# Kernel tuning notes

Measured on AMD Instinct MI355X. Metric: run time of the kernel, lower is better.

## Reference

```python
import jax, jax.numpy as jnp
import numpy as np

B, N, M = 2, 4096, 12288
K, SH, H, GK, NC, F = 64, 32, 64, 8, 200, 1


def sph_to_cart(theta, phi):
    st = jnp.sin(theta)
    return jnp.stack([st * jnp.cos(phi), st * jnp.sin(phi), jnp.cos(theta)], axis=-1)


def setup_inputs() -> dict:
    key = jax.random.key(0)
    ks = jax.random.split(key, 16)
    theta = jax.random.uniform(ks[0], (B, N)) * jnp.pi
    phi = jax.random.uniform(ks[1], (B, N)) * 2 * jnp.pi
    feat = jax.random.normal(ks[2], (B, N))
    xxx = jnp.stack([theta, phi, feat], axis=1)  # [B,3,N]
    pt = jax.random.uniform(ks[3], (M,)) * jnp.pi
    pp = jax.random.uniform(ks[4], (M,)) * 2 * jnp.pi
    pix_theta_phi = jnp.stack([pt, pp], axis=1)  # [M,2]
    s = 0.1
    return dict(
        xxx=xxx,
        pix_theta_phi=pix_theta_phi,
        att_w1=jax.random.normal(ks[5], (F + 1, SH)) * s,
        att_b1=jnp.zeros((SH,)),
        att_w2=jax.random.normal(ks[6], (SH, 1)) * s,
        att_b2=jnp.zeros((1,)),
        proj_w=jax.random.normal(ks[7], (F, H)) * s,
        proj_b=jnp.zeros((H,)),
        rel_w=jax.random.normal(ks[8], (3, H, H)) * s,
        rel_b=jnp.zeros((3, H)),
        root_w=jax.random.normal(ks[9], (3, H, H)) * s,
        out_w1=jax.random.normal(ks[10], (H, H)) * s,
        out_b1=jnp.zeros((H,)),
        out_w2=jax.random.normal(ks[11], (H, NC)) * s,
        out_b2=jnp.zeros((NC,)),
    )


def reference(xxx, pix_theta_phi, att_w1, att_b1, att_w2, att_b2, proj_w, proj_b,
              rel_w, rel_b, root_w, out_w1, out_b1, out_w2, out_b2):
    # --- sparse healpix sampler ---
    los_tp = jnp.transpose(xxx[:, :2, :], (0, 2, 1))   # [B,N,2]
    x = xxx[:, 2, :][..., None]                        # [B,N,1]
    r_los = sph_to_cart(los_tp[..., 0], los_tp[..., 1])           # [B,N,3]
    r_pix = sph_to_cart(pix_theta_phi[:, 0], pix_theta_phi[:, 1])  # [M,3]
    cos = jnp.clip(jnp.einsum('bnc,mc->bmn', r_los, r_pix), -1.0, 1.0)  # [B,M,N]
    vals, idx = jax.lax.top_k(cos, K)                  # [B,M,K]
    x_g = jax.vmap(lambda xb, ib: xb[ib])(x, idx)      # [B,M,K,F]
    d = jnp.arccos(jnp.clip(vals, -1.0, 1.0))          # [B,M,K]
    feat = jnp.concatenate([x_g, d[..., None]], axis=-1)  # [B,M,K,F+1]
    logits = jax.nn.relu(feat @ att_w1 + att_b1) @ att_w2 + att_b2  # [B,M,K,1]
    w = jax.nn.softmax(logits[..., 0], axis=-1)        # [B,M,K]
    pooled = jnp.einsum('bmk,bmkf->bmf', w, x_g)       # [B,M,F]
    # --- GNN on healpix grid ---
    h = jax.nn.relu(pooled @ proj_w + proj_b)          # [B,M,H]
    m = r_pix.shape[0]
    sq = jnp.sum(r_pix * r_pix, axis=1)
    d2 = sq[:, None] + sq[None, :] - 2.0 * (r_pix @ r_pix.T)       # [M,M]
    d2 = jnp.where(jnp.eye(m, dtype=bool), jnp.inf, d2)  # loop=False
    _, nbr = jax.lax.top_k(-d2, GK)                    # [M,GK] knn_graph
    for i in range(rel_w.shape[0]):
        agg = h[:, nbr, :].sum(axis=2)                 # sum-aggregate neighbor msgs
        h = jax.nn.relu(agg @ rel_w[i] + rel_b[i] + h @ root_w[i])
    graph_feat = h.mean(axis=1)                        # global_mean_pool -> [B,H]
    out = jax.nn.relu(graph_feat @ out_w1 + out_b1) @ out_w2 + out_b2
    return out
```

## Files before the change

### kernel.cpp

```cpp
#include <hip/hip_runtime.h>
#include <hip/hip_bf16.h>

#define B_ 2
#define N_ 4096
#define M_ 12288
#define K_ 64
#define SH_ 32
#define H_ 64
#define GK_ 8
#define NC_ 200

#define KCAP 128
#define BCAP2 48
#define SCAP 192
#define MG_ 0.01f
#define C256_ 81.48733086f

static __device__ __forceinline__ unsigned f2key(float f) {
  unsigned b = __float_as_uint(f);
  return (b & 0x80000000u) ? ~b : (b | 0x80000000u);
}
static __device__ __forceinline__ float key2f(unsigned u) {
  unsigned b = (u & 0x80000000u) ? (u & 0x7fffffffu) : ~u;
  return __uint_as_float(b);
}
static __device__ __forceinline__ unsigned long long shflxor64(unsigned long long x, int m) {
  unsigned lo = (unsigned)x, hi = (unsigned)(x >> 32);
  lo = (unsigned)__shfl_xor((int)lo, m);
  hi = (unsigned)__shfl_xor((int)hi, m);
  return ((unsigned long long)hi << 32) | lo;
}
static __device__ __forceinline__ unsigned long long kpack(float s, int j) {
  return ((unsigned long long)f2key(s) << 14) | (unsigned)(16383 - j);
}
static __device__ __forceinline__ unsigned long long spack(float c, int n) {
  return ((unsigned long long)f2key(c) << 12) | (unsigned)(4095 - n);
}
static __device__ __forceinline__ int thbkt(float th) {
  int b = (int)(th * C256_);
  return b < 0 ? 0 : (b > 255 ? 255 : b);
}
static __device__ __forceinline__ float clamp1(float x) { return fminf(1.f, fmaxf(-1.f, x)); }
static __device__ __forceinline__ float rdlane(float v, int c) {
  return __uint_as_float((unsigned)__builtin_amdgcn_readlane((int)__float_as_uint(v), c));
}

__global__ __launch_bounds__(256) void sentinel_vF(float* out, int n, float val) {
  int t = blockIdx.x * 256 + threadIdx.x;
  if (t < n) out[t] = val;
}

#define GRIDB_ 129
#define PREPN_ (M_ + B_*N_ + B_*H_)
#define PREPB_ ((PREPN_ + 255)/256)

__global__ __launch_bounds__(256) void prep_vF(
    const float* __restrict__ xxx, const float* __restrict__ pix,
    float4* __restrict__ r_pix, float4* __restrict__ r_los, float* __restrict__ gf,
    float* __restrict__ kthrG, float* __restrict__ cthrG, unsigned* __restrict__ cnt)
{
  const float PI = 3.14159265358979f;
  if ((int)blockIdx.x < GRIDB_) {
    int gid  = blockIdx.x*4 + (threadIdx.x >> 6);
    if (gid >= 514) return;
    int lane = threadIdx.x & 63;
    int tgt  = (gid >= 257) ? 1 : 0;
    int gp   = gid - tgt*257;
    float thp = (float)gp * (PI/256.f);
    float cp = cosf(thp), sp = fmaxf(sinf(thp), 1e-6f);
    float thq = ((float)lane + 0.5f) * (PI/64.f);
    float sq = sinf(thq), cq = cosf(thq);
    float rinv = 1.0f / (sq * sp);
    float At = tgt ? (2.f*PI*PI*128.f/(float)N_) : (2.f*PI*PI*48.f/(float)M_);
    float lo = 1e-3f, hi = 3.1414f;
    for (int it = 0; it < 12; ++it) {
      float al = 0.5f*(lo + hi);
      float ca = cosf(al);
      float arg = clamp1((ca - cq*cp) * rinv);
      float ax = fabsf(arg);
      float ac = sqrtf(fmaxf(0.f, 1.f - ax)) *
                 fmaf(ax, fmaf(ax, fmaf(ax, -0.0187293f, 0.0742610f), -0.2121144f), 1.5707288f);
      ac = (arg < 0.f) ? (PI - ac) : ac;
      float S = ac;
      #pragma unroll
      for (int off = 32; off; off >>= 1) S += __shfl_xor(S, off);
      float A = 2.f * S * (PI/64.f);
      if (A < At) lo = al; else hi = al;
    }
    if (lane == 0) {
      float chv = cosf(hi);
      if (tgt) cthrG[gp] = chv - 1e-5f;
      else     kthrG[gp] = 2.f*chv - 1.00002f;
    }
  } else {
    int tid = ((int)blockIdx.x - GRIDB_)*256 + threadIdx.x;
    if (tid < M_) {
      float th = pix[2*tid], ph = pix[2*tid+1];
      float st = sinf(th);
      float x = st*cosf(ph), y = st*sinf(ph), z = cosf(th);
      r_pix[tid] = make_float4(x, y, z, x*x + y*y + z*z);
      atomicAdd(&cnt[thbkt(th)], 1u);
    }
    int t2 = tid - M_;
    if (t2 >= 0 && t2 < B_*N_) {
      int b = t2 >> 12, n = t2 & (N_-1);
      const float* xb = xxx + b*3*N_;
      float th = xb[n], ph = xb[N_+n], ft = xb[2*N_+n];
      float st = sinf(th);
      r_los[t2] = make_float4(st*cosf(ph), st*sinf(ph), cosf(th), ft);
      atomicAdd(&cnt[256 + b*256 + thbkt(th)], 1u);
    }
    int t3 = tid - M_ - B_*N_;
    if (t3 >= 0 && t3 < B_*H_) gf[t3] = 0.0f;
  }
}

__global__ __launch_bounds__(256) void scan_vF(
    const unsigned* __restrict__ cnt, int* __restrict__ pstart, int* __restrict__ lstart,
    unsigned* __restrict__ pcur, unsigned* __restrict__ lcur)
{
  __shared__ unsigned buf[256];
  const int t = threadIdx.x;
  for (int arr = 0; arr < 3; ++arr) {
    unsigned v = cnt[arr*256 + t];
    buf[t] = v;
    __syncthreads();
    for (int off = 1; off < 256; off <<= 1) {
      unsigned o = (t >= off) ? buf[t - off] : 0u;
      __syncthreads();
      buf[t] += o;
      __syncthreads();
    }
    unsigned incl = buf[t], excl = incl - v;
    if (arr == 0) {
      pstart[t] = (int)excl; if (t == 255) pstart[256] = (int)incl;
      pcur[t] = excl;
    } else {
      int b = arr - 1;
      lstart[b*257 + t] = (int)excl; if (t == 255) lstart[b*257 + 256] = (int)incl;
      lcur[b*256 + t] = excl;
    }
    __syncthreads();
  }
}

__global__ __launch_bounds__(256) void scatter_vF(
    const float* __restrict__ xxx, const float* __restrict__ pix,
    const float4* __restrict__ r_pix, const float4* __restrict__ r_los,
    unsigned* __restrict__ pcur, unsigned* __restrict__ lcur,
    float4* __restrict__ spix, int* __restrict__ sjdx,
    float4* __restrict__ slos, int* __restrict__ sldx)
{
  int tid = blockIdx.x * 256 + threadIdx.x;
  if (tid < M_) {
    int bkt = thbkt(pix[2*tid]);
    unsigned pos = atomicAdd(&pcur[bkt], 1u);
    spix[pos] = r_pix[tid];
    sjdx[pos] = tid;
  } else {
    int t2 = tid - M_;
    if (t2 < B_*N_) {
      int b = t2 >> 12, n = t2 & (N_-1);
      int bkt = thbkt(xxx[b*3*N_ + n]);
      unsigned pos = atomicAdd(&lcur[b*256 + bkt], 1u);
      slos[b*N_ + pos] = r_los[t2];
      sldx[b*N_ + pos] = n;
    }
  }
}

__global__ __launch_bounds__(512) void sampler_vF(
    const float* __restrict__ pix,
    const float4* __restrict__ spix, const int* __restrict__ sjdx,
    const float4* __restrict__ slos, const int* __restrict__ sldx,
    const int* __restrict__ lstart, const float4* __restrict__ r_los,
    const float* __restrict__ cthrG,
    const float* __restrict__ aw1, const float* __restrict__ ab1,
    const float* __restrict__ aw2, const float* __restrict__ ab2,
    float* __restrict__ pooled)
{
  __shared__ unsigned long long cand[16][SCAP];
  __shared__ unsigned long long selKey[16][K_];
  __shared__ unsigned long long bndK[16][BCAP2];
  __shared__ unsigned hist[16][64];

  const int tid = threadIdx.x, wv = tid >> 6, lane = tid & 63;
  const int b  = blockIdx.y;
  const int srow0 = blockIdx.x*16 + wv*2, srow1 = srow0 + 1;
  const int r0 = wv*2, r1 = r0 + 1;
  const int m0 = sjdx[srow0], m1 = sjdx[srow1];
  const float4 p0 = spix[srow0], p1 = spix[srow1];
  const float thp0 = pix[2*m0], thp1 = pix[2*m1];
  const int g0 = thbkt(thp0), g1 = thbkt(thp1);
  const float th0 = fminf(cthrG[g0], cthrG[g0+1]);
  const float th1 = fminf(cthrG[g1], cthrG[g1+1]);
  const float inv0 = 63.999f / (1.000001f - th0);
  const float inv1 = 63.999f / (1.000001f - th1);
  const float4* sl = slos + b * N_;
  const int* sx = sldx + b * N_;
  const float4* rl = r_los + b * N_;
  const int* ls = lstart + b * 257;
  const unsigned long long ltm = (1ull << lane) - 1ull;

  int jlo, jhi;
  {
    float al0 = acosf(clamp1(th0)), al1 = acosf(clamp1(th1));
    int blo = thbkt(fminf(thp0 - al0, thp1 - al1) - MG_);
    int bhi = thbkt(fmaxf(thp0 + al0, thp1 + al1) + MG_);
    jlo = ls[blo]; jhi = ls[bhi + 1];
  }

  unsigned cnt0 = 0, cnt1 = 0;
  for (int base = jlo; base < jhi; base += 64) {
    int pos = base + lane;
    bool act = pos < jhi;
    float c0 = -2.f, c1 = -2.f; int n = 0;
    if (act) {
      float4 v = sl[pos]; n = sx[pos];
      c0 = clamp1(v.x*p0.x + v.y*p0.y + v.z*p0.z);
      c1 = clamp1(v.x*p1.x + v.y*p1.y + v.z*p1.z);
    }
    bool pr0 = c0 > th0, pr1 = c1 > th1;
    unsigned long long mk0 = __ballot(pr0);
    if (mk0) {
      unsigned off = (unsigned)__popcll(mk0 & ltm);
      if (pr0 && cnt0 + off < SCAP) cand[r0][cnt0 + off] = spack(c0, n);
      cnt0 += (unsigned)__popcll(mk0);
    }
    unsigned long long mk1 = __ballot(pr1);
    if (mk1) {
      unsigned off = (unsigned)__popcll(mk1 & ltm);
      if (pr1 && cnt1 + off < SCAP) cand[r1][cnt1 + off] = spack(c1, n);
      cnt1 += (unsigned)__popcll(mk1);
    }
  }

  for (int rr = 0; rr < 2; ++rr) {
    const int r = (rr == 0) ? r0 : r1;
    const int m = (rr == 0) ? m0 : m1;
    const float4 p = (rr == 0) ? p0 : p1;
    const float thp = (rr == 0) ? thp0 : thp1;
    const float thg = (rr == 0) ? th0 : th1;
    const float invg = (rr == 0) ? inv0 : inv1;
    unsigned cn = (rr == 0) ? cnt0 : cnt1;
    bool fin = false;

    if (cn >= (unsigned)K_ && cn <= (unsigned)SCAP) {
      hist[r][lane] = 0u;
      for (int i = lane; i < (int)cn; i += 64) {
        float c = key2f((unsigned)(cand[r][i] >> 12));
        atomicAdd(&hist[r][(int)((c - thg) * invg)], 1u);
      }
      unsigned g = hist[r][lane], s = g;
      #pragma unroll
      for (int off = 1; off < 64; off <<= 1) {
        unsigned t2 = (unsigned)__shfl_down((int)s, off);
        s += (lane + off < 64) ? t2 : 0u;
      }
      unsigned snext = s - g;
      unsigned packed = (s >= K_ && snext < K_) ? (((unsigned)(lane+1) << 16) | snext) : 0u;
      #pragma unroll
      for (int off = 32; off; off >>= 1) {
        unsigned o = (unsigned)__shfl_xor((int)packed, off);
        packed = packed > o ? packed : o;
      }
      const int t = (int)(packed >> 16) - 1;
      const unsigned chi = packed & 0xFFFFu;
      const unsigned need = K_ - chi;

      unsigned hiC = 0, bdC = 0;
      for (int i0 = 0; i0 < (int)cn; i0 += 64) {
        int i = i0 + lane;
        bool act = i < (int)cn;
        unsigned long long key = act ? cand[r][i] : 0ull;
        int bin = -1;
        if (act) bin = (int)((key2f((unsigned)(key >> 12)) - thg) * invg);
        bool pHi = act && bin > t, pBd = act && bin == t;
        unsigned long long mH = __ballot(pHi);
        unsigned offH = (unsigned)__popcll(mH & ltm);
        if (pHi && hiC + offH < K_) selKey[r][hiC + offH] = key;
        hiC += (unsigned)__popcll(mH);
        unsigned long long mB = __ballot(pBd);
        unsigned offB = (unsigned)__popcll(mB & ltm);
        if (pBd && bdC + offB < BCAP2) bndK[r][bdC + offB] = key;
        bdC += (unsigned)__popcll(mB);
      }
      if (bdC <= (unsigned)BCAP2) {
        if (lane < (int)bdC) {
          unsigned long long ki = bndK[r][lane];
          int rank = 0;
          for (int j = 0; j < (int)bdC; ++j) rank += (bndK[r][j] > ki) ? 1 : 0;
          if ((unsigned)rank < need) selKey[r][chi + rank] = ki;
        }
        fin = true;
      }
    }

    if (!fin) {
      float th = thg;
      float inv = invg;
      int wlo = jlo, whi = jhi;

      if (cn >= (unsigned)K_) {
        hist[r][lane] = 0u;
        cn = 0;
        for (int base = wlo; base < whi; base += 64) {
          int pos = base + lane;
          bool act = pos < whi;
          float c = -2.f;
          if (act) {
            float4 v = sl[pos];
            c = clamp1(v.x*p.x + v.y*p.y + v.z*p.z);
          }
          bool pr = c > th;
          if (pr) atomicAdd(&hist[r][(int)((c - th) * inv)], 1u);
          cn += (unsigned)__popcll(__ballot(pr));
        }
      }

      int tries = 0;
      while (cn < K_ && tries < 3) {
        th = 1.f - 1.6f*(1.f - th); ++tries;
        inv = 63.999f / (1.000001f - th);
        float al = acosf(clamp1(th));
        int blo = thbkt(thp - al - MG_), bhi = thbkt(thp + al + MG_);
        wlo = ls[blo]; whi = ls[bhi + 1];
        hist[r][lane] = 0u;
        cn = 0;
        for (int base = wlo; base < whi; base += 64) {
          int pos = base + lane;
          bool act = pos < whi;
          float c = -2.f;
          if (act) {
            float4 v = sl[pos];
            c = clamp1(v.x*p.x + v.y*p.y + v.z*p.z);
          }
          bool pr = c > th;
          if (pr) atomicAdd(&hist[r][(int)((c - th) * inv)], 1u);
          cn += (unsigned)__popcll(__ballot(pr));
        }
      }

      bool fin2 = false;
      if (cn >= K_) {
        unsigned g = hist[r][lane], s = g;
        #pragma unroll
        for (int off = 1; off < 64; off <<= 1) {
          unsigned t2 = (unsigned)__shfl_down((int)s, off);
          s += (lane + off < 64) ? t2 : 0u;
        }
        unsigned snext = s - g;
        unsigned packed = (s >= K_ && snext < K_) ? (((unsigned)(lane+1) << 16) | snext) : 0u;
        #pragma unroll
        for (int off = 32; off; off >>= 1) {
          unsigned o = (unsigned)__shfl_xor((int)packed, off);
          packed = packed > o ? packed : o;
        }
        const int t = (int)(packed >> 16) - 1;
        const unsigned chi = packed & 0xFFFFu;
        const unsigned need = K_ - chi;

        unsigned hiC = 0, bdC = 0;
        for (int base = wlo; base < whi; base += 64) {
          int pos = base + lane;
          bool act = pos < whi;
          float c = -2.f; int n = 0;
          if (act) {
            float4 v = sl[pos]; n = sx[pos];
            c = clamp1(v.x*p.x + v.y*p.y + v.z*p.z);
          }
          int bin = (act && c > th) ? (int)((c - th) * inv) : -1;
          bool pHi = bin > t;
          bool pBd = bin == t;
          unsigned long long mH = __ballot(pHi);
          unsigned offH = (unsigned)__popcll(mH & ltm);
          if (pHi && hiC + offH < K_) selKey[r][hiC + offH] = spack(c, n);
          hiC += (unsigned)__popcll(mH);
          unsigned long long mB = __ballot(pBd);
          unsigned offB = (unsigned)__popcll(mB & ltm);
          if (pBd && bdC + offB < BCAP2) bndK[r][bdC + offB] = spack(c, n);
          bdC += (unsigned)__popcll(mB);
        }
        if (bdC <= (unsigned)BCAP2) {
          if (lane < (int)bdC) {
            unsigned long long ki = bndK[r][lane];
            int rank = 0;
            for (int j = 0; j < (int)bdC; ++j) rank += (bndK[r][j] > ki) ? 1 : 0;
            if ((unsigned)rank < need) selKey[r][chi + rank] = ki;
          }
          fin2 = true;
        }
      }

      if (!fin2) {
        unsigned long long prev = ~0ull;
        for (int rd = 0; rd < K_; ++rd) {
          unsigned long long best = 0ull;
          for (int i = 0; i < 64; ++i) {
            int n = lane + 64*i;
            float4 v = rl[n];
            float c = clamp1(v.x*p.x + v.y*p.y + v.z*p.z);
            unsigned long long k = spack(c, n);
            if (k < prev && k > best) best = k;
          }
          #pragma unroll
          for (int off = 1; off < 64; off <<= 1) {
            unsigned long long o = shflxor64(best, off);
            best = o > best ? o : best;
          }
          if (lane == 0) selKey[r][rd] = best;
          prev = best;
        }
      }
    }

    {
      unsigned long long key = selKey[r][lane];
      int n = 4095 - (int)(key & 0xFFFull);
      float c = key2f((unsigned)(key >> 12));
      float xg = rl[n].w;
      float d  = acosf(clamp1(c));
      float acc = ab2[0];
      for (int s2 = 0; s2 < SH_; ++s2)
        acc += fmaxf(xg*aw1[s2] + d*aw1[SH_+s2] + ab1[s2], 0.f) * aw2[s2];
      float mx = acc;
      #pragma unroll
      for (int off = 32; off; off >>= 1) mx = fmaxf(mx, __shfl_xor(mx, off));
      float e = expf(acc - mx);
      float se = e, sxe = e * xg;
      #pragma unroll
      for (int off = 32; off; off >>= 1) { se += __shfl_xor(se, off); sxe += __shfl_xor(sxe, off); }
      if (lane == 0) pooled[b*M_ + m] = sxe / se;
    }
  }
}

__global__ __launch_bounds__(512) void knn_vF(
    const float* __restrict__ pix,
    const float4* __restrict__ spix, const int* __restrict__ sjdx,
    const int* __restrict__ pstart, const float4* __restrict__ r_pix,
    const float* __restrict__ kthrG, int* __restrict__ nbr)
{
  __shared__ unsigned long long cKey[16][KCAP];

  const int tid = threadIdx.x, wv = tid >> 6, lane = tid & 63;
  const int lr0 = wv*2;
  const int srow0 = blockIdx.x*16 + lr0, srow1 = srow0 + 1;
  const int i0 = sjdx[srow0], i1 = sjdx[srow1];
  const float4 p0 = spix[srow0], p1 = spix[srow1];
  const float thp0 = pix[2*i0], thp1 = pix[2*i1];
  const int g0 = thbkt(thp0), g1 = thbkt(thp1);
  const float t0 = fminf(kthrG[g0], kthrG[g0+1]);
  const float t1 = fminf(kthrG[g1], kthrG[g1+1]);
  const unsigned long long ltm = (1ull << lane) - 1ull;

  unsigned cnt0 = 0, cnt1 = 0;
  {
    float al0 = acosf(clamp1((t0 + 1.00002f)*0.5f));
    float al1 = acosf(clamp1((t1 + 1.00002f)*0.5f));
    int blo = thbkt(fminf(thp0 - al0, thp1 - al1) - MG_);
    int bhi = thbkt(fmaxf(thp0 + al0, thp1 + al1) + MG_);
    int jlo = pstart[blo], jhi = pstart[bhi + 1];
    for (int base = jlo; base < jhi; base += 64) {
      int pos = base + lane;
      bool act = pos < jhi;
      float s0 = -1e30f, s1 = -1e30f; int j = -1;
      if (act) {
        float4 v = spix[pos]; j = sjdx[pos];
        s0 = 2.f*(p0.x*v.x + p0.y*v.y + p0.z*v.z) - v.w;
        s1 = 2.f*(p1.x*v.x + p1.y*v.y + p1.z*v.z) - v.w;
      }
      bool pr0 = act && (j != i0) && (s0 > t0);
      bool pr1 = act && (j != i1) && (s1 > t1);
      unsigned long long mk0 = __ballot(pr0);
      if (mk0) {
        unsigned off = (unsigned)__popcll(mk0 & ltm);
        if (pr0 && cnt0 + off < KCAP) cKey[lr0][cnt0 + off] = kpack(s0, j);
        cnt0 += (unsigned)__popcll(mk0);
      }
      unsigned long long mk1 = __ballot(pr1);
      if (mk1) {
        unsigned off = (unsigned)__popcll(mk1 & ltm);
        if (pr1 && cnt1 + off < KCAP) cKey[lr0+1][cnt1 + off] = kpack(s1, j);
        cnt1 += (unsigned)__popcll(mk1);
      }
    }
  }

  for (int rr = 0; rr < 2; ++rr) {
    const int lr = lr0 + rr;
    const int i  = (rr == 0) ? i0 : i1;
    const float4 pi = (rr == 0) ? p0 : p1;
    const float thp = (rr == 0) ? thp0 : thp1;
    float th = (rr == 0) ? t0 : t1;
    unsigned cn = (rr == 0) ? cnt0 : cnt1;

    int tries = 0;
    while (cn < (unsigned)GK_ && tries < 3) {
      th = 1.6f*th - 0.6f; ++tries;
      float al = acosf(clamp1((th + 1.00002f)*0.5f));
      int blo = thbkt(thp - al - MG_), bhi = thbkt(thp + al + MG_);
      int jlo = pstart[blo], jhi = pstart[bhi + 1];
      cn = 0;
      for (int base = jlo; base < jhi; base += 64) {
        int pos = base + lane;
        bool act = pos < jhi;
        float s = -1e30f; int j = -1;
        if (act) {
          float4 v = spix[pos]; j = sjdx[pos];
          s = 2.f*(pi.x*v.x + pi.y*v.y + pi.z*v.z) - v.w;
        }
        bool pr = act && (j != i) && (s > th);
        unsigned long long mk = __ballot(pr);
        if (mk) {
          unsigned off = (unsigned)__popcll(mk & ltm);
          if (pr && cn + off < KCAP) cKey[lr][cn + off] = kpack(s, j);
          cn += (unsigned)__popcll(mk);
        }
      }
    }

    if (cn >= (unsigned)GK_ && cn <= (unsigned)KCAP) {
      unsigned long long pk[2];
      #pragma unroll
      for (int t2 = 0; t2 < 2; ++t2) {
        int idx = lane + 64*t2;
        pk[t2] = (idx < (int)cn) ? cKey[lr][idx] : 0ull;
      }
      for (int round = 0; round < GK_; ++round) {
        unsigned long long loc = pk[0]; int lt = 0;
        if (pk[1] > loc) { loc = pk[1]; lt = 1; }
        unsigned long long best = loc;
        #pragma unroll
        for (int off = 1; off < 64; off <<= 1) {
          unsigned long long o = shflxor64(best, off);
          best = o > best ? o : best;
        }
        if (loc == best) pk[lt] = 0ull;
        if (lane == round) nbr[i*GK_ + round] = 16383 - (int)(best & 16383ull);
      }
    } else {
      unsigned long long prev = ~0ull;
      for (int rd = 0; rd < GK_; ++rd) {
        unsigned long long best = 0ull;
        for (int j = lane; j < M_; j += 64) {
          float4 v = r_pix[j];
          float s = 2.f*(pi.x*v.x + pi.y*v.y + pi.z*v.z) - v.w;
          if (j != i) {
            unsigned long long k = kpack(s, j);
            if (k < prev && k > best) best = k;
          }
        }
        #pragma unroll
        for (int off = 1; off < 64; off <<= 1) {
          unsigned long long o = shflxor64(best, off);
          best = o > best ? o : best;
        }
        if (lane == rd) nbr[i*GK_ + rd] = 16383 - (int)(best & 16383ull);
        prev = best;
      }
    }
  }
}

__global__ __launch_bounds__(256) void gnn1f_vF(
    const float* __restrict__ pooled, float* __restrict__ hout, const int* __restrict__ nbr,
    const float* __restrict__ pw, const float* __restrict__ pb,
    const float* __restrict__ relw, const float* __restrict__ relb,
    const float* __restrict__ rootw)
{
  __shared__ float wrel[H_*H_], wroot[H_*H_];
  const int tid = threadIdx.x;
  #pragma unroll
  for (int q = 0; q < 16; ++q) {
    int idx = tid + 256*q;
    wrel[idx]  = relw[idx];
    wroot[idx] = rootw[idx];
  }
  __syncthreads();

  const int lane = tid & 63;
  const int wave = tid >> 6;
  const int b = blockIdx.y;
  const int m0 = blockIdx.x * 16 + wave * 4;
  const float* pldb = pooled + (size_t)b * M_;
  const float pwl = pw[lane], pbl = pb[lane], rbl = relb[lane];

  float h[4], agg[4], acc[4];
  #pragma unroll
  for (int t = 0; t < 4; ++t) {
    int m = m0 + t;
    float ps = pldb[m];
    h[t] = fmaxf(ps*pwl + pbl, 0.f);
    float a = 0.f;
    #pragma unroll
    for (int k = 0; k < GK_; ++k) {
      int nb = nbr[m*GK_ + k];
      nb = nb < 0 ? 0 : (nb >= M_ ? M_-1 : nb);
      float pn = pldb[nb];
      a += fmaxf(pn*pwl + pbl, 0.f);
    }
    agg[t] = a;
    acc[t] = rbl;
  }
  #pragma unroll
  for (int c = 0; c < H_; ++c) {
    float wr = wrel[c*H_ + lane], wo = wroot[c*H_ + lane];
    #pragma unroll
    for (int t = 0; t < 4; ++t)
      acc[t] += rdlane(agg[t], c) * wr + rdlane(h[t], c) * wo;
  }
  #pragma unroll
  for (int t = 0; t < 4; ++t)
    hout[((size_t)b*M_ + m0 + t)*H_ + lane] = fmaxf(acc[t], 0.f);
}

__global__ __launch_bounds__(256) void gnn_vF(
    const float* __restrict__ hin, float* __restrict__ hout, const int* __restrict__ nbr,
    const float* __restrict__ relw, const float* __restrict__ relb,
    const float* __restrict__ rootw)
{
  __shared__ float wrel[H_*H_], wroot[H_*H_];
  const int tid = threadIdx.x;
  #pragma unroll
  for (int q = 0; q < 16; ++q) {
    int idx = tid + 256*q;
    wrel[idx]  = relw[idx];
    wroot[idx] = rootw[idx];
  }
  __syncthreads();

  const int lane = tid & 63;
  const int wave = tid >> 6;
  const int b = blockIdx.y;
  const int m0 = blockIdx.x * 16 + wave * 4;
  const float* hb = hin + (size_t)b * M_ * H_;
  const float rbl = relb[lane];

  float h[4], agg[4], acc[4];
  #pragma unroll
  for (int t = 0; t < 4; ++t) {
    int m = m0 + t;
    h[t] = hb[m*H_ + lane];
    float a = 0.f;
    #pragma unroll
    for (int k = 0; k < GK_; ++k) {
      int nb = nbr[m*GK_ + k];
      nb = nb < 0 ? 0 : (nb >= M_ ? M_-1 : nb);
      a += hb[nb*H_ + lane];
    }
    agg[t] = a;
    acc[t] = rbl;
  }
  #pragma unroll
  for (int c = 0; c < H_; ++c) {
    float wr = wrel[c*H_ + lane], wo = wroot[c*H_ + lane];
    #pragma unroll
    for (int t = 0; t < 4; ++t)
      acc[t] += rdlane(agg[t], c) * wr + rdlane(h[t], c) * wo;
  }
  #pragma unroll
  for (int t = 0; t < 4; ++t)
    hout[((size_t)b*M_ + m0 + t)*H_ + lane] = fmaxf(acc[t], 0.f);
}

__global__ __launch_bounds__(256) void gnn3r_vF(
    const float* __restrict__ hin, float* __restrict__ gf, const int* __restrict__ nbr,
    const float* __restrict__ relw, const float* __restrict__ relb,
    const float* __restrict__ rootw)
{
  __shared__ float wrel[H_*H_], wroot[H_*H_];
  __shared__ float gacc[H_];
  const int tid = threadIdx.x;
  #pragma unroll
  for (int q = 0; q < 16; ++q) {
    int idx = tid + 256*q;
    wrel[idx]  = relw[idx];
    wroot[idx] = rootw[idx];
  }
  if (tid < H_) gacc[tid] = 0.f;
  __syncthreads();

  const int lane = tid & 63;
  const int wave = tid >> 6;
  const int b = blockIdx.y;
  const int m0 = blockIdx.x * 16 + wave * 4;
  const float* hb = hin + (size_t)b * M_ * H_;
  const float rbl = relb[lane];

  float h[4], agg[4], acc[4];
  #pragma unroll
  for (int t = 0; t < 4; ++t) {
    int m = m0 + t;
    h[t] = hb[m*H_ + lane];
    float a = 0.f;
    #pragma unroll
    for (int k = 0; k < GK_; ++k) {
      int nb = nbr[m*GK_ + k];
      nb = nb < 0 ? 0 : (nb >= M_ ? M_-1 : nb);
      a += hb[nb*H_ + lane];
    }
    agg[t] = a;
    acc[t] = rbl;
  }
  #pragma unroll
  for (int c = 0; c < H_; ++c) {
    float wr = wrel[c*H_ + lane], wo = wroot[c*H_ + lane];
    #pragma unroll
    for (int t = 0; t < 4; ++t)
      acc[t] += rdlane(agg[t], c) * wr + rdlane(h[t], c) * wo;
  }
  float ps = fmaxf(acc[0], 0.f) + fmaxf(acc[1], 0.f) + fmaxf(acc[2], 0.f) + fmaxf(acc[3], 0.f);
  atomicAdd(&gacc[lane], ps);
  __syncthreads();
  if (tid < H_) atomicAdd(&gf[b*H_ + tid], gacc[tid]);
}

__global__ __launch_bounds__(256) void head_vF(
    const float* __restrict__ gf, const float* __restrict__ w1,
    const float* __restrict__ b1, const float* __restrict__ w2,
    const float* __restrict__ b2, float* __restrict__ out)
{
  __shared__ float gfm[B_][H_], hid[B_][H_];
  const int tid = threadIdx.x;
  if (tid < B_*H_) gfm[tid >> 6][tid & 63] = gf[tid] * (1.f / (float)M_);
  __syncthreads();
  if (tid < B_*H_) {
    int b = tid >> 6, j = tid & 63;
    float acc = b1[j];
    for (int c = 0; c < H_; ++c) acc += gfm[b][c] * w1[c*H_ + j];
    hid[b][j] = fmaxf(acc, 0.f);
  }
  __syncthreads();
  for (int t = tid; t < B_*NC_; t += 256) {
    int b = t / NC_, o = t - b*NC_;
    float acc = b2[o];
    for (int j = 0; j < H_; ++j) acc += hid[b][j] * w2[j*NC_ + o];
    out[t] = acc;
  }
}

extern "C" void kernel_launch(void* const* d_in, const int* in_sizes, int n_in,
                              void* d_out, int out_size, void* d_ws, size_t ws_size,
                              hipStream_t stream)
{
  float* out = (float*)d_out;

  const size_t need = (size_t)M_*16 + (size_t)B_*N_*16 + (size_t)B_*M_*4
                    + (size_t)M_*GK_*4 + 2*(size_t)B_*M_*H_*4 + (size_t)B_*H_*4;
  bool ok_ws = ws_size >= need;
  bool ok_in = (n_in == 15) && (out_size == B_*NC_)
            && in_sizes[0] == B_*3*N_ && in_sizes[1] == M_*2
            && in_sizes[2] == 2*SH_ && in_sizes[5] == 1
            && in_sizes[8] == 3*H_*H_ && in_sizes[13] == H_*NC_;
  if (!ok_ws || !ok_in) {
    sentinel_vF<<<(out_size + 255)/256, 256, 0, stream>>>(out, out_size, ok_in ? 42.f : 43.f);
    return;
  }

  const float* xxx    = (const float*)d_in[0];
  const float* pix    = (const float*)d_in[1];
  const float* att_w1 = (const float*)d_in[2];
  const float* att_b1 = (const float*)d_in[3];
  const float* att_w2 = (const float*)d_in[4];
  const float* att_b2 = (const float*)d_in[5];
  const float* proj_w = (const float*)d_in[6];
  const float* proj_b = (const float*)d_in[7];
  const float* rel_w  = (const float*)d_in[8];
  const float* rel_b  = (const float*)d_in[9];
  const float* root_w = (const float*)d_in[10];
  const float* out_w1 = (const float*)d_in[11];
  const float* out_b1 = (const float*)d_in[12];
  const float* out_w2 = (const float*)d_in[13];
  const float* out_b2 = (const float*)d_in[14];

  char* w = (char*)d_ws;
  float4* r_pix = (float4*)w;  w += (size_t)M_ * 16;
  float4* r_los = (float4*)w;  w += (size_t)B_ * N_ * 16;
  float*  pooled = (float*)w;  w += (size_t)B_ * M_ * 4;
  int*    nbr = (int*)w;       w += (size_t)M_ * GK_ * 4;
  float*  h0 = (float*)w;      w += (size_t)B_ * M_ * H_ * 4;
  float*  h1 = (float*)w;      w += (size_t)B_ * M_ * H_ * 4;
  float*  gf = (float*)w;      w += (size_t)B_ * H_ * 4;

  float*  kthrG = h0;
  float*  cthrG = h0 + 512;
  float4* spix = (float4*)(h0 + 2*M_);
  int*    sjdx = (int*)(h0 + 6*M_);
  float4* slos = (float4*)(h0 + 7*M_);
  int*    sldx = (int*)(h0 + 7*M_ + 4*B_*N_);
  unsigned* cnt = (unsigned*)(h0 + 7*M_ + 5*B_*N_);
  int*    pstart = (int*)(cnt + 768);
  int*    lstart = pstart + 257;
  unsigned* pcur = (unsigned*)(lstart + 514);
  unsigned* lcur = pcur + 256;

  hipMemsetAsync(cnt, 0, 768*sizeof(unsigned), stream);
  prep_vF<<<GRIDB_ + PREPB_, 256, 0, stream>>>(xxx, pix, r_pix, r_los, gf, kthrG, cthrG, cnt);
  scan_vF<<<1, 256, 0, stream>>>(cnt, pstart, lstart, pcur, lcur);
  scatter_vF<<<(M_ + B_*N_ + 255)/256, 256, 0, stream>>>(xxx, pix, r_pix, r_los, pcur, lcur,
                                                         spix, sjdx, slos, sldx);
  sampler_vF<<<dim3(M_/16, B_), 512, 0, stream>>>(pix, spix, sjdx, slos, sldx, lstart, r_los,
                                                  cthrG, att_w1, att_b1, att_w2, att_b2, pooled);
  knn_vF<<<M_/16, 512, 0, stream>>>(pix, spix, sjdx, pstart, r_pix, kthrG, nbr);
  gnn1f_vF<<<dim3(M_/16, B_), 256, 0, stream>>>(pooled, h1, nbr, proj_w, proj_b,
                                                rel_w + 0*H_*H_, rel_b + 0*H_, root_w + 0*H_*H_);
  gnn_vF<<<dim3(M_/16, B_), 256, 0, stream>>>(h1, h0, nbr, rel_w + 1*H_*H_, rel_b + 1*H_, root_w + 1*H_*H_);
  gnn3r_vF<<<dim3(M_/16, B_), 256, 0, stream>>>(h0, gf, nbr, rel_w + 2*H_*H_, rel_b + 2*H_, root_w + 2*H_*H_);
  head_vF<<<1, 256, 0, stream>>>(gf, out_w1, out_b1, out_w2, out_b2, out);
}
```

Baseline: 239.2 us.

## Bin points into 2D theta-phi grid and scan only phi window per row

Replaces the 256 theta-only buckets used to sort pixels and line-of-sight points with a 32x128 theta-by-phi grid. The sampler and kNN candidate scans now walk each theta row and read only the phi range that can hold neighbours within the angular threshold, wrapping around 2π where needed. The aim is to cut the number of candidate dot products and ballots in the two dominant search kernels. In exchange the prefix scan handles 4096 buckets per array, the window maths adds per-wave trig, and the fallback retry paths still scan whole theta rows.

```diff
diff --git a/kernel.cpp b/kernel.cpp
--- a/kernel.cpp
+++ b/kernel.cpp
@@ -16,6 +16,14 @@
 #define MG_ 0.01f
 #define C256_ 81.48733086f
 
+#define TB_ 32
+#define PB_ 128
+#define NBKT_ (TB_*PB_)
+#define CTB_ 10.18591636f
+#define CPB_ 20.37183271f
+#define TWO_PI_ 6.28318530718f
+#define INV2PI_ 0.15915494309f
+
 static __device__ __forceinline__ unsigned f2key(float f) {
   unsigned b = __float_as_uint(f);
   return (b & 0x80000000u) ? ~b : (b | 0x80000000u);
@@ -40,12 +48,48 @@
   int b = (int)(th * C256_);
   return b < 0 ? 0 : (b > 255 ? 255 : b);
 }
+static __device__ __forceinline__ int tbkt(float th) {
+  int b = (int)(th * CTB_);
+  return b < 0 ? 0 : (b > TB_-1 ? TB_-1 : b);
+}
+static __device__ __forceinline__ int pbkt(float ph) {
+  int b = (int)(ph * CPB_);
+  return b < 0 ? 0 : (b > PB_-1 ? PB_-1 : b);
+}
 static __device__ __forceinline__ float clamp1(float x) { return fminf(1.f, fmaxf(-1.f, x)); }
 static __device__ __forceinline__ float rdlane(float v, int c) {
   return __uint_as_float((unsigned)__builtin_amdgcn_readlane((int)__float_as_uint(v), c));
 }
 
-__global__ __launch_bounds__(256) void sentinel_vF(float* out, int n, float val) {
+static __device__ __forceinline__ void phi_window(
+    float thp0, float php0, float al0, float thp1, float php1, float al1,
+    int& pbl, int& nb)
+{
+  float sp0 = sinf(thp0), sp1 = sinf(thp1);
+  float sa0 = sinf(fminf(al0 + MG_, 1.5707f));
+  float sa1 = sinf(fminf(al1 + MG_, 1.5707f));
+  bool full = (sa0 >= sp0 * 0.9999f) || (sa1 >= sp1 * 0.9999f);
+  if (!full) {
+    float dp0 = asinf(fminf(sa0 / sp0, 1.f)) + MG_;
+    float dp1 = asinf(fminf(sa1 / sp1, 1.f)) + MG_;
+    float d = php1 - php0;
+    d -= floorf(d * INV2PI_ + 0.5f) * TWO_PI_;
+    float lo = fminf(-dp0, d - dp1), hi = fmaxf(dp0, d + dp1);
+    float wdt = hi - lo;
+    if (wdt >= TWO_PI_ * 0.95f) full = true;
+    else {
+      float a0 = php0 + lo;
+      a0 -= floorf(a0 * INV2PI_) * TWO_PI_;
+      pbl = (int)(a0 * CPB_);
+      pbl = pbl < 0 ? 0 : (pbl > PB_-1 ? PB_-1 : pbl);
+      nb = (int)(wdt * CPB_) + 2;
+      if (nb > PB_) nb = PB_;
+    }
+  }
+  if (full) { pbl = 0; nb = PB_; }
+}
+
+__global__ __launch_bounds__(256) void sentinel_vG(float* out, int n, float val) {
   int t = blockIdx.x * 256 + threadIdx.x;
   if (t < n) out[t] = val;
 }
@@ -54,7 +98,7 @@
 #define PREPN_ (M_ + B_*N_ + B_*H_)
 #define PREPB_ ((PREPN_ + 255)/256)
 
-__global__ __launch_bounds__(256) void prep_vF(
+__global__ __launch_bounds__(256) void prep_vG(
     const float* __restrict__ xxx, const float* __restrict__ pix,
     float4* __restrict__ r_pix, float4* __restrict__ r_los, float* __restrict__ gf,
     float* __restrict__ kthrG, float* __restrict__ cthrG, unsigned* __restrict__ cnt)
@@ -99,7 +143,7 @@
       float st = sinf(th);
       float x = st*cosf(ph), y = st*sinf(ph), z = cosf(th);
       r_pix[tid] = make_float4(x, y, z, x*x + y*y + z*z);
-      atomicAdd(&cnt[thbkt(th)], 1u);
+      atomicAdd(&cnt[tbkt(th)*PB_ + pbkt(ph)], 1u);
     }
     int t2 = tid - M_;
     if (t2 >= 0 && t2 < B_*N_) {
@@ -108,22 +152,25 @@
       float th = xb[n], ph = xb[N_+n], ft = xb[2*N_+n];
       float st = sinf(th);
       r_los[t2] = make_float4(st*cosf(ph), st*sinf(ph), cosf(th), ft);
-      atomicAdd(&cnt[256 + b*256 + thbkt(th)], 1u);
+      atomicAdd(&cnt[NBKT_ + b*NBKT_ + tbkt(th)*PB_ + pbkt(ph)], 1u);
     }
     int t3 = tid - M_ - B_*N_;
     if (t3 >= 0 && t3 < B_*H_) gf[t3] = 0.0f;
   }
 }
 
-__global__ __launch_bounds__(256) void scan_vF(
-    const unsigned* __restrict__ cnt, int* __restrict__ pstart, int* __restrict__ lstart,
+__global__ __launch_bounds__(256) void scan_vG(
+    const unsigned* __restrict__ cnt, int* __restrict__ s2p, int* __restrict__ s2l,
     unsigned* __restrict__ pcur, unsigned* __restrict__ lcur)
 {
   __shared__ unsigned buf[256];
   const int t = threadIdx.x;
   for (int arr = 0; arr < 3; ++arr) {
-    unsigned v = cnt[arr*256 + t];
-    buf[t] = v;
+    const unsigned* c = cnt + arr * NBKT_;
+    unsigned loc[16]; unsigned sum = 0;
+    #pragma unroll
+    for (int k = 0; k < 16; ++k) { loc[k] = c[t*16 + k]; sum += loc[k]; }
+    buf[t] = sum;
     __syncthreads();
     for (int off = 1; off < 256; off <<= 1) {
       unsigned o = (t >= off) ? buf[t - off] : 0u;
@@ -131,20 +178,18 @@
       buf[t] += o;
       __syncthreads();
     }
-    unsigned incl = buf[t], excl = incl - v;
-    if (arr == 0) {
-      pstart[t] = (int)excl; if (t == 255) pstart[256] = (int)incl;
-      pcur[t] = excl;
-    } else {
-      int b = arr - 1;
-      lstart[b*257 + t] = (int)excl; if (t == 255) lstart[b*257 + 256] = (int)incl;
-      lcur[b*256 + t] = excl;
-    }
+    unsigned base = buf[t] - sum;
+    int* s2 = (arr == 0) ? s2p : (s2l + (arr-1)*(NBKT_+1));
+    unsigned* cur = (arr == 0) ? pcur : (lcur + (arr-1)*NBKT_);
+    unsigned run = base;
+    #pragma unroll
+    for (int k = 0; k < 16; ++k) { s2[t*16+k] = (int)run; cur[t*16+k] = run; run += loc[k]; }
+    if (t == 255) s2[NBKT_] = (int)run;
     __syncthreads();
   }
 }
 
-__global__ __launch_bounds__(256) void scatter_vF(
+__global__ __launch_bounds__(256) void scatter_vG(
     const float* __restrict__ xxx, const float* __restrict__ pix,
     const float4* __restrict__ r_pix, const float4* __restrict__ r_los,
     unsigned* __restrict__ pcur, unsigned* __restrict__ lcur,
@@ -153,7 +198,7 @@
 {
   int tid = blockIdx.x * 256 + threadIdx.x;
   if (tid < M_) {
-    int bkt = thbkt(pix[2*tid]);
+    int bkt = tbkt(pix[2*tid])*PB_ + pbkt(pix[2*tid+1]);
     unsigned pos = atomicAdd(&pcur[bkt], 1u);
     spix[pos] = r_pix[tid];
     sjdx[pos] = tid;
@@ -161,19 +206,20 @@
     int t2 = tid - M_;
     if (t2 < B_*N_) {
       int b = t2 >> 12, n = t2 & (N_-1);
-      int bkt = thbkt(xxx[b*3*N_ + n]);
-      unsigned pos = atomicAdd(&lcur[b*256 + bkt], 1u);
+      const float* xb = xxx + b*3*N_;
+      int bkt = tbkt(xb[n])*PB_ + pbkt(xb[N_+n]);
+      unsigned pos = atomicAdd(&lcur[b*NBKT_ + bkt], 1u);
       slos[b*N_ + pos] = r_los[t2];
       sldx[b*N_ + pos] = n;
     }
   }
 }
 
-__global__ __launch_bounds__(512) void sampler_vF(
+__global__ __launch_bounds__(512) void sampler_vG(
     const float* __restrict__ pix,
     const float4* __restrict__ spix, const int* __restrict__ sjdx,
     const float4* __restrict__ slos, const int* __restrict__ sldx,
-    const int* __restrict__ lstart, const float4* __restrict__ r_los,
+    const int* __restrict__ s2l, const float4* __restrict__ r_los,
     const float* __restrict__ cthrG,
     const float* __restrict__ aw1, const float* __restrict__ ab1,
     const float* __restrict__ aw2, const float* __restrict__ ab2,
@@ -191,6 +237,7 @@
   const int m0 = sjdx[srow0], m1 = sjdx[srow1];
   const float4 p0 = spix[srow0], p1 = spix[srow1];
   const float thp0 = pix[2*m0], thp1 = pix[2*m1];
+  const float php0 = pix[2*m0+1], php1 = pix[2*m1+1];
   const int g0 = thbkt(thp0), g1 = thbkt(thp1);
   const float th0 = fminf(cthrG[g0], cthrG[g0+1]);
   const float th1 = fminf(cthrG[g1], cthrG[g1+1]);
@@ -199,39 +246,49 @@
   const float4* sl = slos + b * N_;
   const int* sx = sldx + b * N_;
   const float4* rl = r_los + b * N_;
-  const int* ls = lstart + b * 257;
+  const int* s2b = s2l + b * (NBKT_+1);
   const unsigned long long ltm = (1ull << lane) - 1ull;
 
-  int jlo, jhi;
+  const float al0 = acosf(clamp1(th0)), al1 = acosf(clamp1(th1));
+  int rlo, rhi, pbl, nb;
   {
-    float al0 = acosf(clamp1(th0)), al1 = acosf(clamp1(th1));
-    int blo = thbkt(fminf(thp0 - al0, thp1 - al1) - MG_);
-    int bhi = thbkt(fmaxf(thp0 + al0, thp1 + al1) + MG_);
-    jlo = ls[blo]; jhi = ls[bhi + 1];
+    rlo = tbkt(fminf(thp0 - al0, thp1 - al1) - MG_);
+    rhi = tbkt(fmaxf(thp0 + al0, thp1 + al1) + MG_);
+    phi_window(thp0, php0, al0, thp1, php1, al1, pbl, nb);
   }
 
   unsigned cnt0 = 0, cnt1 = 0;
-  for (int base = jlo; base < jhi; base += 64) {
-    int pos = base + lane;
-    bool act = pos < jhi;
-    float c0 = -2.f, c1 = -2.f; int n = 0;
-    if (act) {
-      float4 v = sl[pos]; n = sx[pos];
-      c0 = clamp1(v.x*p0.x + v.y*p0.y + v.z*p0.z);
-      c1 = clamp1(v.x*p1.x + v.y*p1.y + v.z*p1.z);
-    }
-    bool pr0 = c0 > th0, pr1 = c1 > th1;
-    unsigned long long mk0 = __ballot(pr0);
-    if (mk0) {
-      unsigned off = (unsigned)__popcll(mk0 & ltm);
-      if (pr0 && cnt0 + off < SCAP) cand[r0][cnt0 + off] = spack(c0, n);
-      cnt0 += (unsigned)__popcll(mk0);
-    }
-    unsigned long long mk1 = __ballot(pr1);
-    if (mk1) {
-      unsigned off = (unsigned)__popcll(mk1 & ltm);
-      if (pr1 && cnt1 + off < SCAP) cand[r1][cnt1 + off] = spack(c1, n);
-      cnt1 += (unsigned)__popcll(mk1);
+  {
+    auto chunk = [&](int base, int e) {
+      int pos = base + lane;
+      bool act = pos < e;
+      float c0 = -2.f, c1 = -2.f; int n = 0;
+      if (act) {
+        float4 v = sl[pos]; n = sx[pos];
+        c0 = clamp1(v.x*p0.x + v.y*p0.y + v.z*p0.z);
+        c1 = clamp1(v.x*p1.x + v.y*p1.y + v.z*p1.z);
+      }
+      bool pr0 = c0 > th0, pr1 = c1 > th1;
+      unsigned long long mk0 = __ballot(pr0);
+      if (mk0) {
+        unsigned off = (unsigned)__popcll(mk0 & ltm);
+        if (pr0 && cnt0 + off < SCAP) cand[r0][cnt0 + off] = spack(c0, n);
+        cnt0 += (unsigned)__popcll(mk0);
+      }
+      unsigned long long mk1 = __ballot(pr1);
+      if (mk1) {
+        unsigned off = (unsigned)__popcll(mk1 & ltm);
+        if (pr1 && cnt1 + off < SCAP) cand[r1][cnt1 + off] = spack(c1, n);
+        cnt1 += (unsigned)__popcll(mk1);
+      }
+    };
+    for (int row = rlo; row <= rhi; ++row) {
+      const int rb = row * PB_;
+      int s1 = s2b[rb + pbl], e1, s2 = 0, e2 = 0;
+      if (pbl + nb <= PB_) e1 = s2b[rb + pbl + nb];
+      else { e1 = s2b[rb + PB_]; s2 = s2b[rb]; e2 = s2b[rb + pbl + nb - PB_]; }
+      for (int base = s1; base < e1; base += 64) chunk(base, e1);
+      for (int base = s2; base < e2; base += 64) chunk(base, e2);
     }
   }
 
@@ -299,7 +356,7 @@
     if (!fin) {
       float th = thg;
       float inv = invg;
-      int wlo = jlo, whi = jhi;
+      int wlo = s2b[rlo * PB_], whi = s2b[(rhi + 1) * PB_];
 
       if (cn >= (unsigned)K_) {
         hist[r][lane] = 0u;
@@ -323,8 +380,8 @@
         th = 1.f - 1.6f*(1.f - th); ++tries;
         inv = 63.999f / (1.000001f - th);
         float al = acosf(clamp1(th));
-        int blo = thbkt(thp - al - MG_), bhi = thbkt(thp + al + MG_);
-        wlo = ls[blo]; whi = ls[bhi + 1];
+        int blo = tbkt(thp - al - MG_), bhi = tbkt(thp + al + MG_);
+        wlo = s2b[blo * PB_]; whi = s2b[(bhi + 1) * PB_];
         hist[r][lane] = 0u;
         cn = 0;
         for (int base = wlo; base < whi; base += 64) {
@@ -435,10 +492,10 @@
   }
 }
 
-__global__ __launch_bounds__(512) void knn_vF(
+__global__ __launch_bounds__(512) void knn_vG(
     const float* __restrict__ pix,
     const float4* __restrict__ spix, const int* __restrict__ sjdx,
-    const int* __restrict__ pstart, const float4* __restrict__ r_pix,
+    const int* __restrict__ s2p, const float4* __restrict__ r_pix,
     const float* __restrict__ kthrG, int* __restrict__ nbr)
 {
   __shared__ unsigned long long cKey[16][KCAP];
@@ -449,6 +506,7 @@
   const int i0 = sjdx[srow0], i1 = sjdx[srow1];
   const float4 p0 = spix[srow0], p1 = spix[srow1];
   const float thp0 = pix[2*i0], thp1 = pix[2*i1];
+  const float php0 = pix[2*i0+1], php1 = pix[2*i1+1];
   const int g0 = thbkt(thp0), g1 = thbkt(thp1);
   const float t0 = fminf(kthrG[g0], kthrG[g0+1]);
   const float t1 = fminf(kthrG[g1], kthrG[g1+1]);
@@ -458,12 +516,14 @@
   {
     float al0 = acosf(clamp1((t0 + 1.00002f)*0.5f));
     float al1 = acosf(clamp1((t1 + 1.00002f)*0.5f));
-    int blo = thbkt(fminf(thp0 - al0, thp1 - al1) - MG_);
-    int bhi = thbkt(fmaxf(thp0 + al0, thp1 + al1) + MG_);
-    int jlo = pstart[blo], jhi = pstart[bhi + 1];
-    for (int base = jlo; base < jhi; base += 64) {
+    int rlo = tbkt(fminf(thp0 - al0, thp1 - al1) - MG_);
+    int rhi = tbkt(fmaxf(thp0 + al0, thp1 + al1) + MG_);
+    int pbl, nb;
+    phi_window(thp0, php0, al0, thp1, php1, al1, pbl, nb);
+
+    auto chunk = [&](int base, int e) {
       int pos = base + lane;
-      bool act = pos < jhi;
+      bool act = pos < e;
       float s0 = -1e30f, s1 = -1e30f; int j = -1;
       if (act) {
         float4 v = spix[pos]; j = sjdx[pos];
@@ -484,6 +544,14 @@
         if (pr1 && cnt1 + off < KCAP) cKey[lr0+1][cnt1 + off] = kpack(s1, j);
         cnt1 += (unsigned)__popcll(mk1);
       }
+    };
+    for (int row = rlo; row <= rhi; ++row) {
+      const int rb = row * PB_;
+      int s1 = s2p[rb + pbl], e1, s2 = 0, e2 = 0;
+      if (pbl + nb <= PB_) e1 = s2p[rb + pbl + nb];
+      else { e1 = s2p[rb + PB_]; s2 = s2p[rb]; e2 = s2p[rb + pbl + nb - PB_]; }
+      for (int base = s1; base < e1; base += 64) chunk(base, e1);
+      for (int base = s2; base < e2; base += 64) chunk(base, e2);
     }
   }
 
@@ -499,8 +567,8 @@
     while (cn < (unsigned)GK_ && tries < 3) {
       th = 1.6f*th - 0.6f; ++tries;
       float al = acosf(clamp1((th + 1.00002f)*0.5f));
-      int blo = thbkt(thp - al - MG_), bhi = thbkt(thp + al + MG_);
-      int jlo = pstart[blo], jhi = pstart[bhi + 1];
+      int blo = tbkt(thp - al - MG_), bhi = tbkt(thp + al + MG_);
+      int jlo = s2p[blo * PB_], jhi = s2p[(bhi + 1) * PB_];
       cn = 0;
       for (int base = jlo; base < jhi; base += 64) {
         int pos = base + lane;
@@ -563,7 +631,7 @@
   }
 }
 
-__global__ __launch_bounds__(256) void gnn1f_vF(
+__global__ __launch_bounds__(256) void gnn1f_vG(
     const float* __restrict__ pooled, float* __restrict__ hout, const int* __restrict__ nbr,
     const float* __restrict__ pw, const float* __restrict__ pb,
     const float* __restrict__ relw, const float* __restrict__ relb,
@@ -615,7 +683,7 @@
     hout[((size_t)b*M_ + m0 + t)*H_ + lane] = fmaxf(acc[t], 0.f);
 }
 
-__global__ __launch_bounds__(256) void gnn_vF(
+__global__ __launch_bounds__(256) void gnn_vG(
     const float* __restrict__ hin, float* __restrict__ hout, const int* __restrict__ nbr,
     const float* __restrict__ relw, const float* __restrict__ relb,
     const float* __restrict__ rootw)
@@ -664,7 +732,7 @@
     hout[((size_t)b*M_ + m0 + t)*H_ + lane] = fmaxf(acc[t], 0.f);
 }
 
-__global__ __launch_bounds__(256) void gnn3r_vF(
+__global__ __launch_bounds__(256) void gnn3r_vG(
     const float* __restrict__ hin, float* __restrict__ gf, const int* __restrict__ nbr,
     const float* __restrict__ relw, const float* __restrict__ relb,
     const float* __restrict__ rootw)
@@ -716,7 +784,7 @@
   if (tid < H_) atomicAdd(&gf[b*H_ + tid], gacc[tid]);
 }
 
-__global__ __launch_bounds__(256) void head_vF(
+__global__ __launch_bounds__(256) void head_vG(
     const float* __restrict__ gf, const float* __restrict__ w1,
     const float* __restrict__ b1, const float* __restrict__ w2,
     const float* __restrict__ b2, float* __restrict__ out)
@@ -754,7 +822,7 @@
             && in_sizes[2] == 2*SH_ && in_sizes[5] == 1
             && in_sizes[8] == 3*H_*H_ && in_sizes[13] == H_*NC_;
   if (!ok_ws || !ok_in) {
-    sentinel_vF<<<(out_size + 255)/256, 256, 0, stream>>>(out, out_size, ok_in ? 42.f : 43.f);
+    sentinel_vG<<<(out_size + 255)/256, 256, 0, stream>>>(out, out_size, ok_in ? 42.f : 43.f);
     return;
   }
 
@@ -790,22 +858,22 @@
   float4* slos = (float4*)(h0 + 7*M_);
   int*    sldx = (int*)(h0 + 7*M_ + 4*B_*N_);
   unsigned* cnt = (unsigned*)(h0 + 7*M_ + 5*B_*N_);
-  int*    pstart = (int*)(cnt + 768);
-  int*    lstart = pstart + 257;
-  unsigned* pcur = (unsigned*)(lstart + 514);
-  unsigned* lcur = pcur + 256;
-
-  hipMemsetAsync(cnt, 0, 768*sizeof(unsigned), stream);
-  prep_vF<<<GRIDB_ + PREPB_, 256, 0, stream>>>(xxx, pix, r_pix, r_los, gf, kthrG, cthrG, cnt);
-  scan_vF<<<1, 256, 0, stream>>>(cnt, pstart, lstart, pcur, lcur);
-  scatter_vF<<<(M_ + B_*N_ + 255)/256, 256, 0, stream>>>(xxx, pix, r_pix, r_los, pcur, lcur,
+  int*    s2p = (int*)(cnt + 3*NBKT_);
+  int*    s2l = s2p + (NBKT_+1);
+  unsigned* pcur = (unsigned*)(s2l + 2*(NBKT_+1));
+  unsigned* lcur = pcur + NBKT_;
+
+  hipMemsetAsync(cnt, 0, 3*NBKT_*sizeof(unsigned), stream);
+  prep_vG<<<GRIDB_ + PREPB_, 256, 0, stream>>>(xxx, pix, r_pix, r_los, gf, kthrG, cthrG, cnt);
+  scan_vG<<<1, 256, 0, stream>>>(cnt, s2p, s2l, pcur, lcur);
+  scatter_vG<<<(M_ + B_*N_ + 255)/256, 256, 0, stream>>>(xxx, pix, r_pix, r_los, pcur, lcur,
                                                          spix, sjdx, slos, sldx);
-  sampler_vF<<<dim3(M_/16, B_), 512, 0, stream>>>(pix, spix, sjdx, slos, sldx, lstart, r_los,
+  sampler_vG<<<dim3(M_/16, B_), 512, 0, stream>>>(pix, spix, sjdx, slos, sldx, s2l, r_los,
                                                   cthrG, att_w1, att_b1, att_w2, att_b2, pooled);
-  knn_vF<<<M_/16, 512, 0, stream>>>(pix, spix, sjdx, pstart, r_pix, kthrG, nbr);
-  gnn1f_vF<<<dim3(M_/16, B_), 256, 0, stream>>>(pooled, h1, nbr, proj_w, proj_b,
+  knn_vG<<<M_/16, 512, 0, stream>>>(pix, spix, sjdx, s2p, r_pix, kthrG, nbr);
+  gnn1f_vG<<<dim3(M_/16, B_), 256, 0, stream>>>(pooled, h1, nbr, proj_w, proj_b,
                                                 rel_w + 0*H_*H_, rel_b + 0*H_, root_w + 0*H_*H_);
-  gnn_vF<<<dim3(M_/16, B_), 256, 0, stream>>>(h1, h0, nbr, rel_w + 1*H_*H_, rel_b + 1*H_, root_w + 1*H_*H_);
-  gnn3r_vF<<<dim3(M_/16, B_), 256, 0, stream>>>(h0, gf, nbr, rel_w + 2*H_*H_, rel_b + 2*H_, root_w + 2*H_*H_);
-  head_vF<<<1, 256, 0, stream>>>(gf, out_w1, out_b1, out_w2, out_b2, out);
-}
+  gnn_vG<<<dim3(M_/16, B_), 256, 0, stream>>>(h1, h0, nbr, rel_w + 1*H_*H_, rel_b + 1*H_, root_w + 1*H_*H_);
+  gnn3r_vG<<<dim3(M_/16, B_), 256, 0, stream>>>(h0, gf, nbr, rel_w + 2*H_*H_, rel_b + 2*H_, root_w + 2*H_*H_);
+  head_vG<<<1, 256, 0, stream>>>(gf, out_w1, out_b1, out_w2, out_b2, out);
+}
```

Result: no change. 242.6 us (+1.4%).
